# Kernel optimization log

Measured on AMD Instinct MI355X. Metric: run time of the kernel, lower is better.

## Reference

```python
import jax, jax.numpy as jnp
import numpy as np

NUM_QUBITS = 22
NUM_LAYERS = 4
DIM = 2 ** NUM_QUBITS


def _apply_1q(state, U, q):
    # state: flat [2^n]; apply 2x2 unitary U on wire q (wire 0 = most significant)
    s = state.reshape(2 ** q, 2, -1)
    return jnp.einsum('ab,ibj->iaj', U, s).reshape(-1)


def _apply_cnot_adj(state, q):
    # CNOT with control q, target q+1 (adjacent wires)
    s = state.reshape(2 ** q, 2, 2, -1)
    s = jnp.stack([s[:, 0], s[:, 1, ::-1]], axis=1)
    return s.reshape(-1)


def _rot_mats(theta_x, theta_y, theta_z):
    cx = jnp.cos(theta_x / 2).astype(jnp.complex64)
    sx = jnp.sin(theta_x / 2).astype(jnp.complex64)
    RX = jnp.stack([jnp.stack([cx, -1j * sx]), jnp.stack([-1j * sx, cx])])
    cy = jnp.cos(theta_y / 2).astype(jnp.complex64)
    sy = jnp.sin(theta_y / 2).astype(jnp.complex64)
    RY = jnp.stack([jnp.stack([cy, -sy]), jnp.stack([sy, cy])])
    tz = theta_z.astype(jnp.complex64)
    zero = jnp.zeros((), jnp.complex64)
    RZ = jnp.stack([jnp.stack([jnp.exp(-1j * tz / 2), zero]),
                    jnp.stack([zero, jnp.exp(1j * tz / 2)])])
    return RX, RY, RZ


def _circuit(params, state):
    for l in range(NUM_LAYERS):
        for q in range(NUM_QUBITS):
            RX, RY, RZ = _rot_mats(params[l, q, 0], params[l, q, 1], params[l, q, 2])
            state = _apply_1q(state, RX, q)
            state = _apply_1q(state, RY, q)
            state = _apply_1q(state, RZ, q)
        for q in range(NUM_QUBITS - 1):
            state = _apply_cnot_adj(state, q)
    # <Z_q> for each qubit
    probs = jnp.abs(state) ** 2
    expvals = []
    for q in range(NUM_QUBITS):
        p = probs.reshape(2 ** q, 2, -1)
        expvals.append(p[:, 0].sum() - p[:, 1].sum())
    return jnp.stack(expvals).astype(jnp.float32)


def setup_inputs() -> dict:
    key = jax.random.key(0)
    k1, k2, k3 = jax.random.split(key, 3)
    params = jax.random.normal(k1, (NUM_LAYERS, NUM_QUBITS, 3), dtype=jnp.float32)
    state_re = jax.random.normal(k2, (DIM,), dtype=jnp.float32)
    state_im = jax.random.normal(k3, (DIM,), dtype=jnp.float32)
    return {"params": params, "state_re": state_re, "state_im": state_im}


def reference(params, state_re, state_im):
    state = (state_re + 1j * state_im).astype(jnp.complex64)
    state = state / jnp.sqrt(jnp.sum(jnp.abs(state) ** 2))
    return _circuit(params, state)
```

## Files before the change

kernel.cpp:

```cpp
#include <hip/hip_runtime.h>
#include <math.h>

#define NQ 22
#define DIM (1u << NQ)

typedef float v2f __attribute__((ext_vector_type(2)));


__device__ __forceinline__ unsigned igray(unsigned x) {
  x ^= x >> 1; x ^= x >> 2; x ^= x >> 4; x ^= x >> 8; x ^= x >> 16;
  return x;
}

__global__ void k_gates(const float* __restrict__ params, float* __restrict__ U) {
  int t = blockIdx.x * blockDim.x + threadIdx.x;
  if (t >= 88) return;
  const float* p = params + t * 3;
  double hx = 0.5 * (double)p[0], hy = 0.5 * (double)p[1], hz = 0.5 * (double)p[2];
  double cx = cos(hx), sx = sin(hx);
  double cy = cos(hy), sy = sin(hy);
  double cz = cos(hz), sz = sin(hz);
  double m00r = cy * cx, m00i = sy * sx;
  double m01r = -sy * cx, m01i = -cy * sx;
  double m10r = sy * cx, m10i = -cy * sx;
  double m11r = cy * cx, m11i = -sy * sx;
  float* o = U + t * 8;
  o[0] = (float)(cz * m00r + sz * m00i); o[1] = (float)(cz * m00i - sz * m00r);
  o[2] = (float)(cz * m01r + sz * m01i); o[3] = (float)(cz * m01i - sz * m01r);
  o[4] = (float)(cz * m10r - sz * m10i); o[5] = (float)(cz * m10i + sz * m10r);
  o[6] = (float)(cz * m11r - sz * m11i); o[7] = (float)(cz * m11i + sz * m11r);
}

template <int NP>
__device__ __forceinline__ void apply_bit0(v2f RE[NP], v2f IM[NP], const float* __restrict__ u) {
  float u0 = u[0], u1 = u[1], u2 = u[2], u3 = u[3], u4 = u[4], u5 = u[5], u6 = u[6], u7 = u[7];
#pragma unroll
  for (int k = 0; k < NP; ++k) {
    float a0r = RE[k].x, a0i = IM[k].x, a1r = RE[k].y, a1i = IM[k].y;
    float n0r = u0 * a0r - u1 * a0i + u2 * a1r - u3 * a1i;
    float n0i = u0 * a0i + u1 * a0r + u2 * a1i + u3 * a1r;
    float n1r = u4 * a0r - u5 * a0i + u6 * a1r - u7 * a1i;
    float n1i = u4 * a0i + u5 * a0r + u6 * a1i + u7 * a1r;
    RE[k].x = n0r; IM[k].x = n0i; RE[k].y = n1r; IM[k].y = n1i;
  }
}

template <int NP, int PB>
__device__ __forceinline__ void apply_bitP(v2f RE[NP], v2f IM[NP], const float* __restrict__ u) {
  float u0 = u[0], u1 = u[1], u2 = u[2], u3 = u[3], u4 = u[4], u5 = u[5], u6 = u[6], u7 = u[7];
#pragma unroll
  for (int m = 0; m < NP / 2; ++m) {
    int k0 = ((m >> PB) << (PB + 1)) | (m & ((1 << PB) - 1));
    int k1 = k0 | (1 << PB);
    v2f a0r = RE[k0], a0i = IM[k0], a1r = RE[k1], a1i = IM[k1];
    v2f n0r = u0 * a0r - u1 * a0i + u2 * a1r - u3 * a1i;
    v2f n0i = u0 * a0i + u1 * a0r + u2 * a1i + u3 * a1r;
    v2f n1r = u4 * a0r - u5 * a0i + u6 * a1r - u7 * a1i;
    v2f n1i = u4 * a0i + u5 * a0r + u6 * a1i + u7 * a1r;
    RE[k0] = n0r; IM[k0] = n0i; RE[k1] = n1r; IM[k1] = n1i;
  }
}

__device__ __forceinline__ void apply4p(v2f RE[8], v2f IM[8], const float* __restrict__ U,
                                        int l, int wtop) {
  const float* base = U + ((l * 22 + wtop) << 3);
  apply_bit0<8>(RE, IM, base);
  apply_bitP<8, 0>(RE, IM, base - 8);
  apply_bitP<8, 1>(RE, IM, base - 16);
  apply_bitP<8, 2>(RE, IM, base - 24);
}

template <typename WI, typename RI>
__device__ __forceinline__ void xchgP(float2* lds2, v2f RE[8], v2f IM[8], WI wi, RI ri) {
  __syncthreads();
#pragma unroll
  for (int d = 0; d < 16; ++d) {
    float2 a;
    if (d & 1) a = make_float2(RE[d >> 1].y, IM[d >> 1].y);
    else       a = make_float2(RE[d >> 1].x, IM[d >> 1].x);
    lds2[wi(d)] = a;
  }
  __syncthreads();
#pragma unroll
  for (int d = 0; d < 16; ++d) {
    float2 a = lds2[ri(d)];
    if (d & 1) { RE[d >> 1].y = a.x; IM[d >> 1].y = a.y; }
    else       { RE[d >> 1].x = a.x; IM[d >> 1].x = a.y; }
  }
}

__global__ __launch_bounds__(256, 4) void k_passA(const float* __restrict__ srcRe,
                                                  const float* __restrict__ srcIm,
                                                  const float2* __restrict__ src2,
                                                  float2* __restrict__ dst,
                                                  const float* __restrict__ U,
                                                  int layer, int first) {
  __shared__ float2 lds2[4096];
  const int t = threadIdx.x;
  const unsigned bid = blockIdx.x;
  const unsigned H = (bid & 7u) * (gridDim.x >> 3) + (bid >> 3);
  v2f RE[8], IM[8];
  if (first) {
    const unsigned jbase = (H << 12) | ((unsigned)t << 4);
    const float4* r4 = (const float4*)(srcRe + jbase);
    const float4* i4 = (const float4*)(srcIm + jbase);
#pragma unroll
    for (int k = 0; k < 4; ++k) {
      float4 r = r4[k], m = i4[k];
      RE[2 * k].x     = r.x; RE[2 * k].y     = r.y;
      IM[2 * k].x     = m.x; IM[2 * k].y     = m.y;
      RE[2 * k + 1].x = r.z; RE[2 * k + 1].y = r.w;
      IM[2 * k + 1].x = m.z; IM[2 * k + 1].y = m.w;
    }
  } else {
    const float4* s4 = (const float4*)(src2 + (((size_t)H << 12) | ((size_t)t << 4)));
#pragma unroll
    for (int k = 0; k < 8; ++k) {
      float4 a = s4[k];
      RE[k].x = a.x; IM[k].x = a.y;
      RE[k].y = a.z; IM[k].y = a.w;
    }
  }
  auto wA = [&](int d) { unsigned j = ((unsigned)t << 4) | (unsigned)d; return (int)(j ^ (j >> 4)); };
  auto rB = [&](int d) { unsigned j = (((unsigned)t >> 4) << 8) | ((unsigned)d << 4) | ((unsigned)t & 15); return (int)(j ^ (j >> 4)); };
  auto rC = [&](int d) { unsigned j = ((unsigned)d << 8) | (unsigned)t; return (int)(j ^ (j >> 4)); };

  apply4p(RE, IM, U, layer, 21);
  xchgP(lds2, RE, IM, wA, rB);
  apply4p(RE, IM, U, layer, 17);
  xchgP(lds2, RE, IM, rB, rC);
  apply4p(RE, IM, U, layer, 13);
  float2* dp = dst + (((size_t)H << 3) | (unsigned)(t & 7));
#pragma unroll
  for (int d = 0; d < 16; ++d) {
    float2 a;
    if (d & 1) a = make_float2(RE[d >> 1].y, IM[d >> 1].y);
    else       a = make_float2(RE[d >> 1].x, IM[d >> 1].x);
    dp[(((size_t)d << 5) | (unsigned)(t >> 3)) << 13] = a;
  }
}


template <bool EV>
__device__ __forceinline__ void passB_core(const float2* __restrict__ src,
                                           const float* __restrict__ U,
                                           float4* lds4, v2f RE[16], v2f IM[16],
                                           unsigned c2, unsigned u6, unsigned mid,
                                           int layer) {
  const float4* sp4 = (const float4*)src + (((size_t)mid << 12) | c2);
#pragma unroll
  for (int k = 0; k < 16; ++k) {
    float4 a = sp4[((unsigned)k << 8) | (u6 << 2)];
    RE[k].x = a.x; RE[k].y = a.z;
    IM[k].x = a.y; IM[k].y = a.w;
  }
  const float* B = U + layer * 22 * 8;
  apply_bitP<16, 0>(RE, IM, B + 3 * 8);
  apply_bitP<16, 1>(RE, IM, B + 2 * 8);
  apply_bitP<16, 2>(RE, IM, B + 1 * 8);
  apply_bitP<16, 3>(RE, IM, B + 0 * 8);
#pragma unroll
  for (int k = 0; k < 16; ++k) {
    unsigned s = ((unsigned)k << 8) | (u6 << 2) | c2;
    s ^= (s >> 6) & 7u;
    lds4[s] = make_float4(RE[k].x, IM[k].x, RE[k].y, IM[k].y);
  }
  __syncthreads();
#pragma unroll
  for (int k = 0; k < 16; ++k) {
    unsigned s = ((unsigned)k << 2) | (u6 << 6) | c2;
    s ^= (s >> 6) & 7u;
    float4 a = lds4[s];
    RE[k].x = a.x; IM[k].x = a.y;
    RE[k].y = a.z; IM[k].y = a.w;
  }
  apply_bitP<16, 0>(RE, IM, B + 9 * 8);
  apply_bitP<16, 1>(RE, IM, B + 8 * 8);
  apply_bitP<16, 2>(RE, IM, B + 7 * 8);
  apply_bitP<16, 3>(RE, IM, B + 6 * 8);
  __syncthreads();
#pragma unroll
  for (int k = 0; k < 16; ++k) {
    unsigned s = ((unsigned)k << 2) | (u6 << 6) | c2;
    s ^= (s >> 6) & 7u;
    lds4[s] = make_float4(RE[k].x, IM[k].x, RE[k].y, IM[k].y);
  }
  __syncthreads();
#pragma unroll
  for (int k = 0; k < 16; ++k) {
    unsigned h = (u6 & 15u) | (((unsigned)k & 3u) << 4) | (((unsigned)k >> 2) << 6) | ((u6 >> 4) << 8);
    unsigned s = (h << 2) | c2;
    s ^= (s >> 6) & 7u;
    float4 a = lds4[s];
    RE[k].x = a.x; IM[k].x = a.y;
    RE[k].y = a.z; IM[k].y = a.w;
  }
  apply_bitP<16, 0>(RE, IM, B + 5 * 8);
  apply_bitP<16, 1>(RE, IM, B + 4 * 8);
}

__global__ __launch_bounds__(256, 2) void k_passB(const float2* __restrict__ src,
                                                  float2* __restrict__ dst,
                                                  const float* __restrict__ U,
                                                  int layer) {
  __shared__ float4 lds4[4096];
  const int t = threadIdx.x;
  const unsigned c2 = (unsigned)(t & 3), u6 = (unsigned)(t >> 2);
  const unsigned bid = blockIdx.x;
  const unsigned mid = (bid & 7u) * (gridDim.x >> 3) + (bid >> 3);
  v2f RE[16], IM[16];
  passB_core<false>(src, U, lds4, RE, IM, c2, u6, mid, layer);
  const unsigned Tb = igray(((u6 & 15u) << 12) | ((u6 >> 4) << 20) | (mid << 3) | (c2 << 1));
  float4* dp4 = (float4*)dst;
#pragma unroll
  for (int k = 0; k < 16; ++k) {
    unsigned a2 = Tb ^ igray((((unsigned)k & 3u) << 16) | (((unsigned)k >> 2) << 18));
    float4 v = (a2 & 1u) ? make_float4(RE[k].y, IM[k].y, RE[k].x, IM[k].x)
                         : make_float4(RE[k].x, IM[k].x, RE[k].y, IM[k].y);
    dp4[a2 >> 1] = v;
  }
}

__global__ __launch_bounds__(256, 2) void k_passB_ev(const float2* __restrict__ src,
                                                     const float* __restrict__ U,
                                                     float* __restrict__ partials,
                                                     int layer) {
  __shared__ float4 lds4[4096];
  const int t = threadIdx.x;
  const unsigned c2 = (unsigned)(t & 3), u6 = (unsigned)(t >> 2);
  const unsigned bid = blockIdx.x;
  const unsigned mid = (bid & 7u) * (gridDim.x >> 3) + (bid >> 3);
  v2f RE[16], IM[16];
  passB_core<true>(src, U, lds4, RE, IM, c2, u6, mid, layer);

  v2f PS[16];
#pragma unroll
  for (int k = 0; k < 16; ++k) PS[k] = RE[k] * RE[k] + IM[k] * IM[k];
  float Tot = 0.f, WA = 0.f;
  v2f B4[8];
#pragma unroll
  for (int k = 0; k < 8; ++k) {
    v2f S = PS[k] + PS[k + 8];
    Tot += S.x + S.y;
    B4[k] = PS[k] - PS[k + 8];
    WA += B4[k].x + B4[k].y;
  }
  v2f B3[4];
  float WB = 0.f;
#pragma unroll
  for (int k = 0; k < 4; ++k) {
    B3[k] = B4[k] - B4[k + 4];
    WB += B3[k].x + B3[k].y;
  }
  v2f B2[2];
  B2[0] = B3[0] - B3[2]; B2[1] = B3[1] - B3[3];
  float WC = (B2[0].x + B2[0].y) + (B2[1].x + B2[1].y);
  v2f B1 = B2[0] - B2[1];
  float W4 = B1.x + B1.y;
  float W5 = B1.x - B1.y;

  unsigned lowT = (mid << 3) | (c2 << 1);
  unsigned y = lowT; y ^= y >> 1; y ^= y >> 2; y ^= y >> 4; y ^= y >> 8;
  unsigned pu = (unsigned)__popc(u6) & 1u;
  float acc[22];
  acc[0] = ((u6 >> 5) & 1u) ? -Tot : Tot;
  {
    unsigned s01 = (unsigned)__popc(u6 >> 4) & 1u;
    acc[1] = s01 ? -Tot : Tot;
    float sg = s01 ? -1.f : 1.f;
    acc[2] = sg * WA; acc[3] = sg * WB; acc[4] = sg * WC; acc[5] = sg * W4;
  }
#pragma unroll
  for (int q = 6; q <= 9; ++q)
    acc[q] = ((unsigned)__popc(u6 >> (9 - q)) & 1u) ? -W4 : W4;
#pragma unroll
  for (int q = 10; q <= 20; ++q)
    acc[q] = (((y >> (21 - q)) ^ pu) & 1u) ? -W4 : W4;
  acc[21] = (((y >> 1) ^ pu) & 1u) ? -W5 : W5;

  __syncthreads();
  float* red = (float*)lds4;
  const int lane = t & 63, wv = t >> 6;
#pragma unroll
  for (int q = 0; q < 22; ++q) {
    float s = acc[q];
    for (int off = 32; off > 0; off >>= 1) s += __shfl_down(s, off, 64);
    if (lane == 0) red[wv * 23 + q] = s;
  }
  {
    float s = Tot;
    for (int off = 32; off > 0; off >>= 1) s += __shfl_down(s, off, 64);
    if (lane == 0) red[wv * 23 + 22] = s;
  }
  __syncthreads();
  if (t < 23) {
    float s = 0.f;
#pragma unroll
    for (int w = 0; w < 4; ++w) s += red[w * 23 + t];
    partials[t * 512 + mid] = s;
  }
}

__global__ void k_final(const float* __restrict__ partials, float* __restrict__ out) {
  __shared__ double res[32];
  const int t = threadIdx.x;
  const int r = t >> 3, l8 = t & 7;
  if (r < 23) {
    double s = 0.0;
    const float* p = partials + r * 512 + l8 * 64;
    for (int k = 0; k < 64; ++k) s += (double)p[k];
    for (int off = 4; off > 0; off >>= 1) s += __shfl_down(s, off, 8);
    if (l8 == 0) res[r] = s;
  }
  __syncthreads();
  if (t < 22) out[t] = (float)(res[t] / res[22]);
}

extern "C" void kernel_launch(void* const* d_in, const int* in_sizes, int n_in,
                              void* d_out, int out_size, void* d_ws, size_t ws_size,
                              hipStream_t stream) {
  const float* params = (const float*)d_in[0];
  const float* sre = (const float*)d_in[1];
  const float* sim = (const float*)d_in[2];
  float* out = (float*)d_out;
  char* ws = (char*)d_ws;
  float* U = (float*)ws;
  float* partials = (float*)(ws + 4096);
  float2* buf0 = (float2*)(ws + 131072);
  float2* buf1 = buf0 + DIM;

  k_gates<<<1, 128, 0, stream>>>(params, U);
  k_passA<<<1024, 256, 0, stream>>>(sre, sim, nullptr, buf0, U, 0, 1);
  k_passB<<<512, 256, 0, stream>>>(buf0, buf1, U, 0);
  for (int l = 1; l < 3; ++l) {
    k_passA<<<1024, 256, 0, stream>>>(nullptr, nullptr, buf1, buf0, U, l, 0);
    k_passB<<<512, 256, 0, stream>>>(buf0, buf1, U, l);
  }
  k_passA<<<1024, 256, 0, stream>>>(nullptr, nullptr, buf1, buf0, U, 3, 0);
  k_passB_ev<<<512, 256, 0, stream>>>(buf0, U, partials, 3);
  k_final<<<1, 256, 0, stream>>>(partials, out);
}
```

Baseline: 206.9 us.

## Restructure passB into smaller 8-amplitude-per-thread tiles with more blocks

Pass B now handles 10 qubits per block in 3-bit stages, with each thread holding 8 amplitude pairs instead of 16. Shared memory halves to 32KB per block, the grid doubles to 1024 blocks and launch bounds allow 4 blocks per CU. The goal is more occupancy and latency hiding for this memory-bound pass. The cost is an extra LDS exchange round with its own syncs, a reworked XOR swizzle, recomputed expectation-value sign bookkeeping, and twice as many partial sums for the final reduction.

```diff
diff --git a/kernel.cpp b/kernel.cpp
--- a/kernel.cpp
+++ b/kernel.cpp
@@ -141,142 +141,125 @@
 }
 
 
-template <bool EV>
-__device__ __forceinline__ void passB_core(const float2* __restrict__ src,
-                                           const float* __restrict__ U,
-                                           float4* lds4, v2f RE[16], v2f IM[16],
-                                           unsigned c2, unsigned u6, unsigned mid,
-                                           int layer) {
-  const float4* sp4 = (const float4*)src + (((size_t)mid << 12) | c2);
-#pragma unroll
-  for (int k = 0; k < 16; ++k) {
-    float4 a = sp4[((unsigned)k << 8) | (u6 << 2)];
-    RE[k].x = a.x; RE[k].y = a.z;
-    IM[k].x = a.y; IM[k].y = a.w;
-  }
-  const float* B = U + layer * 22 * 8;
-  apply_bitP<16, 0>(RE, IM, B + 3 * 8);
-  apply_bitP<16, 1>(RE, IM, B + 2 * 8);
-  apply_bitP<16, 2>(RE, IM, B + 1 * 8);
-  apply_bitP<16, 3>(RE, IM, B + 0 * 8);
-#pragma unroll
-  for (int k = 0; k < 16; ++k) {
-    unsigned s = ((unsigned)k << 8) | (u6 << 2) | c2;
-    s ^= (s >> 6) & 7u;
-    lds4[s] = make_float4(RE[k].x, IM[k].x, RE[k].y, IM[k].y);
-  }
-  __syncthreads();
-#pragma unroll
-  for (int k = 0; k < 16; ++k) {
-    unsigned s = ((unsigned)k << 2) | (u6 << 6) | c2;
-    s ^= (s >> 6) & 7u;
-    float4 a = lds4[s];
-    RE[k].x = a.x; IM[k].x = a.y;
-    RE[k].y = a.z; IM[k].y = a.w;
-  }
-  apply_bitP<16, 0>(RE, IM, B + 9 * 8);
-  apply_bitP<16, 1>(RE, IM, B + 8 * 8);
-  apply_bitP<16, 2>(RE, IM, B + 7 * 8);
-  apply_bitP<16, 3>(RE, IM, B + 6 * 8);
-  __syncthreads();
-#pragma unroll
-  for (int k = 0; k < 16; ++k) {
-    unsigned s = ((unsigned)k << 2) | (u6 << 6) | c2;
-    s ^= (s >> 6) & 7u;
-    lds4[s] = make_float4(RE[k].x, IM[k].x, RE[k].y, IM[k].y);
-  }
-  __syncthreads();
-#pragma unroll
-  for (int k = 0; k < 16; ++k) {
-    unsigned h = (u6 & 15u) | (((unsigned)k & 3u) << 4) | (((unsigned)k >> 2) << 6) | ((u6 >> 4) << 8);
-    unsigned s = (h << 2) | c2;
-    s ^= (s >> 6) & 7u;
-    float4 a = lds4[s];
-    RE[k].x = a.x; IM[k].x = a.y;
-    RE[k].y = a.z; IM[k].y = a.w;
-  }
-  apply_bitP<16, 0>(RE, IM, B + 5 * 8);
-  apply_bitP<16, 1>(RE, IM, B + 4 * 8);
-}
-
-__global__ __launch_bounds__(256, 2) void k_passB(const float2* __restrict__ src,
+__device__ __forceinline__ int phi(unsigned o) {
+  return (int)(o ^ (((o >> 4) & 7u) << 1));
+}
+
+template <typename WI, typename RI>
+__device__ __forceinline__ void xch4(float4* L, v2f RE[8], v2f IM[8], WI wi, RI ri) {
+#pragma unroll
+  for (int k = 0; k < 8; ++k)
+    L[wi(k)] = make_float4(RE[k].x, IM[k].x, RE[k].y, IM[k].y);
+  __syncthreads();
+#pragma unroll
+  for (int k = 0; k < 8; ++k) {
+    float4 a = L[ri(k)];
+    RE[k].x = a.x; IM[k].x = a.y; RE[k].y = a.z; IM[k].y = a.w;
+  }
+  __syncthreads();
+}
+
+__device__ __forceinline__ void passB_core5(const float2* __restrict__ src,
+                                            const float* __restrict__ B,
+                                            float4* lds4, v2f RE[8], v2f IM[8],
+                                            unsigned c1, unsigned u7,
+                                            unsigned mid, unsigned a2) {
+  const float4* sp4 = (const float4*)src + (((size_t)mid << 12) | (u7 << 2) | (a2 << 1) | c1);
+#pragma unroll
+  for (int k = 0; k < 8; ++k) {
+    float4 a = sp4[(unsigned)k << 9];
+    RE[k].x = a.x; IM[k].x = a.y; RE[k].y = a.z; IM[k].y = a.w;
+  }
+  apply_bitP<8, 0>(RE, IM, B + 2 * 8);
+  apply_bitP<8, 1>(RE, IM, B + 1 * 8);
+  apply_bitP<8, 2>(RE, IM, B + 0 * 8);
+  auto w1 = [&](int k) { return phi(((((unsigned)k << 7) | u7) << 1) | c1); };
+  auto r1 = [&](int k) { return phi((((u7 << 3) | (unsigned)k) << 1) | c1); };
+  xch4(lds4, RE, IM, w1, r1);
+  apply_bitP<8, 0>(RE, IM, B + 9 * 8);
+  apply_bitP<8, 1>(RE, IM, B + 8 * 8);
+  apply_bitP<8, 2>(RE, IM, B + 7 * 8);
+  auto r2 = [&](int k) { return phi((((u7 & 7u) | ((unsigned)k << 3) | ((u7 >> 3) << 6)) << 1) | c1); };
+  xch4(lds4, RE, IM, r1, r2);
+  apply_bitP<8, 0>(RE, IM, B + 6 * 8);
+  apply_bitP<8, 1>(RE, IM, B + 5 * 8);
+  apply_bitP<8, 2>(RE, IM, B + 4 * 8);
+  auto r3 = [&](int k) { return phi((((u7 & 63u) | ((unsigned)k << 6) | ((u7 >> 6) << 9)) << 1) | c1); };
+  xch4(lds4, RE, IM, r2, r3);
+  apply_bitP<8, 0>(RE, IM, B + 3 * 8);
+}
+
+__global__ __launch_bounds__(256, 4) void k_passB(const float2* __restrict__ src,
                                                   float2* __restrict__ dst,
                                                   const float* __restrict__ U,
                                                   int layer) {
-  __shared__ float4 lds4[4096];
+  __shared__ float4 lds4[2048];
   const int t = threadIdx.x;
-  const unsigned c2 = (unsigned)(t & 3), u6 = (unsigned)(t >> 2);
+  const unsigned c1 = (unsigned)(t & 1), u7 = (unsigned)(t >> 1);
   const unsigned bid = blockIdx.x;
-  const unsigned mid = (bid & 7u) * (gridDim.x >> 3) + (bid >> 3);
-  v2f RE[16], IM[16];
-  passB_core<false>(src, U, lds4, RE, IM, c2, u6, mid, layer);
-  const unsigned Tb = igray(((u6 & 15u) << 12) | ((u6 >> 4) << 20) | (mid << 3) | (c2 << 1));
+  const unsigned H = (bid & 7u) * (gridDim.x >> 3) + (bid >> 3);
+  const unsigned mid = H >> 1, a2 = H & 1u;
+  v2f RE[8], IM[8];
+  passB_core5(src, U + layer * 22 * 8, lds4, RE, IM, c1, u7, mid, a2);
+  const unsigned Tb = igray(((u7 & 63u) << 12) | ((u7 >> 6) << 21) |
+                            (mid << 3) | (a2 << 2) | (c1 << 1));
   float4* dp4 = (float4*)dst;
 #pragma unroll
-  for (int k = 0; k < 16; ++k) {
-    unsigned a2 = Tb ^ igray((((unsigned)k & 3u) << 16) | (((unsigned)k >> 2) << 18));
-    float4 v = (a2 & 1u) ? make_float4(RE[k].y, IM[k].y, RE[k].x, IM[k].x)
-                         : make_float4(RE[k].x, IM[k].x, RE[k].y, IM[k].y);
-    dp4[a2 >> 1] = v;
-  }
-}
-
-__global__ __launch_bounds__(256, 2) void k_passB_ev(const float2* __restrict__ src,
+  for (int k = 0; k < 8; ++k) {
+    unsigned a2x = Tb ^ igray((unsigned)k << 18);
+    float4 v = (a2x & 1u) ? make_float4(RE[k].y, IM[k].y, RE[k].x, IM[k].x)
+                          : make_float4(RE[k].x, IM[k].x, RE[k].y, IM[k].y);
+    dp4[a2x >> 1] = v;
+  }
+}
+
+__global__ __launch_bounds__(256, 4) void k_passB_ev(const float2* __restrict__ src,
                                                      const float* __restrict__ U,
                                                      float* __restrict__ partials,
                                                      int layer) {
-  __shared__ float4 lds4[4096];
+  __shared__ float4 lds4[2048];
   const int t = threadIdx.x;
-  const unsigned c2 = (unsigned)(t & 3), u6 = (unsigned)(t >> 2);
+  const unsigned c1 = (unsigned)(t & 1), u7 = (unsigned)(t >> 1);
   const unsigned bid = blockIdx.x;
-  const unsigned mid = (bid & 7u) * (gridDim.x >> 3) + (bid >> 3);
-  v2f RE[16], IM[16];
-  passB_core<true>(src, U, lds4, RE, IM, c2, u6, mid, layer);
-
-  v2f PS[16];
-#pragma unroll
-  for (int k = 0; k < 16; ++k) PS[k] = RE[k] * RE[k] + IM[k] * IM[k];
-  float Tot = 0.f, WA = 0.f;
-  v2f B4[8];
-#pragma unroll
-  for (int k = 0; k < 8; ++k) {
-    v2f S = PS[k] + PS[k + 8];
+  const unsigned H = (bid & 7u) * (gridDim.x >> 3) + (bid >> 3);
+  const unsigned mid = H >> 1, a2 = H & 1u;
+  v2f RE[8], IM[8];
+  passB_core5(src, U + layer * 22 * 8, lds4, RE, IM, c1, u7, mid, a2);
+
+  v2f PS[8];
+#pragma unroll
+  for (int k = 0; k < 8; ++k) PS[k] = RE[k] * RE[k] + IM[k] * IM[k];
+  float Tot = 0.f, W20 = 0.f;
+  v2f Ba[4];
+#pragma unroll
+  for (int j = 0; j < 4; ++j) {
+    v2f S = PS[j] + PS[j + 4];
     Tot += S.x + S.y;
-    B4[k] = PS[k] - PS[k + 8];
-    WA += B4[k].x + B4[k].y;
-  }
-  v2f B3[4];
-  float WB = 0.f;
-#pragma unroll
-  for (int k = 0; k < 4; ++k) {
-    B3[k] = B4[k] - B4[k + 4];
-    WB += B3[k].x + B3[k].y;
-  }
-  v2f B2[2];
-  B2[0] = B3[0] - B3[2]; B2[1] = B3[1] - B3[3];
-  float WC = (B2[0].x + B2[0].y) + (B2[1].x + B2[1].y);
-  v2f B1 = B2[0] - B2[1];
-  float W4 = B1.x + B1.y;
-  float W5 = B1.x - B1.y;
-
-  unsigned lowT = (mid << 3) | (c2 << 1);
-  unsigned y = lowT; y ^= y >> 1; y ^= y >> 2; y ^= y >> 4; y ^= y >> 8;
-  unsigned pu = (unsigned)__popc(u6) & 1u;
+    Ba[j] = PS[j] - PS[j + 4];
+    W20 += Ba[j].x + Ba[j].y;
+  }
+  v2f Bb0 = Ba[0] - Ba[2], Bb1 = Ba[1] - Ba[3];
+  float W19 = Bb0.x + Bb0.y + Bb1.x + Bb1.y;
+  v2f Bc = Bb0 - Bb1;
+  float Wk = Bc.x + Bc.y;
+  float Wkb = Bc.x - Bc.y;
+
+  const unsigned s21 = (u7 >> 6) & 1u;
+  const unsigned pu6 = (unsigned)__popc(u7 & 63u) & 1u;
+  unsigned low = (mid << 3) | (a2 << 2) | (c1 << 1);
+  unsigned y = low; y ^= y >> 1; y ^= y >> 2; y ^= y >> 4; y ^= y >> 8;
   float acc[22];
-  acc[0] = ((u6 >> 5) & 1u) ? -Tot : Tot;
   {
-    unsigned s01 = (unsigned)__popc(u6 >> 4) & 1u;
-    acc[1] = s01 ? -Tot : Tot;
-    float sg = s01 ? -1.f : 1.f;
-    acc[2] = sg * WA; acc[3] = sg * WB; acc[4] = sg * WC; acc[5] = sg * W4;
-  }
-#pragma unroll
-  for (int q = 6; q <= 9; ++q)
-    acc[q] = ((unsigned)__popc(u6 >> (9 - q)) & 1u) ? -W4 : W4;
-#pragma unroll
-  for (int q = 10; q <= 20; ++q)
-    acc[q] = (((y >> (21 - q)) ^ pu) & 1u) ? -W4 : W4;
-  acc[21] = (((y >> 1) ^ pu) & 1u) ? -W5 : W5;
+    float sg = s21 ? -1.f : 1.f;
+    acc[0] = sg * Tot; acc[1] = sg * W20; acc[2] = sg * W19; acc[3] = sg * Wk;
+  }
+#pragma unroll
+  for (int q = 4; q <= 8; ++q)
+    acc[q] = (((unsigned)__popc((u7 & 63u) >> (9 - q)) ^ s21) & 1u) ? -Wk : Wk;
+#pragma unroll
+  for (int q = 9; q <= 20; ++q)
+    acc[q] = (((y >> (21 - q)) ^ s21 ^ pu6) & 1u) ? -Wk : Wk;
+  acc[21] = ((y ^ s21 ^ pu6) & 1u) ? -Wkb : Wkb;
 
   __syncthreads();
   float* red = (float*)lds4;
@@ -297,7 +280,7 @@
     float s = 0.f;
 #pragma unroll
     for (int w = 0; w < 4; ++w) s += red[w * 23 + t];
-    partials[t * 512 + mid] = s;
+    partials[t * 1024 + ((mid << 1) | a2)] = s;
   }
 }
 
@@ -307,8 +290,8 @@
   const int r = t >> 3, l8 = t & 7;
   if (r < 23) {
     double s = 0.0;
-    const float* p = partials + r * 512 + l8 * 64;
-    for (int k = 0; k < 64; ++k) s += (double)p[k];
+    const float* p = partials + r * 1024 + l8 * 128;
+    for (int k = 0; k < 128; ++k) s += (double)p[k];
     for (int off = 4; off > 0; off >>= 1) s += __shfl_down(s, off, 8);
     if (l8 == 0) res[r] = s;
   }
@@ -331,12 +314,12 @@
 
   k_gates<<<1, 128, 0, stream>>>(params, U);
   k_passA<<<1024, 256, 0, stream>>>(sre, sim, nullptr, buf0, U, 0, 1);
-  k_passB<<<512, 256, 0, stream>>>(buf0, buf1, U, 0);
+  k_passB<<<1024, 256, 0, stream>>>(buf0, buf1, U, 0);
   for (int l = 1; l < 3; ++l) {
     k_passA<<<1024, 256, 0, stream>>>(nullptr, nullptr, buf1, buf0, U, l, 0);
-    k_passB<<<512, 256, 0, stream>>>(buf0, buf1, U, l);
+    k_passB<<<1024, 256, 0, stream>>>(buf0, buf1, U, l);
   }
   k_passA<<<1024, 256, 0, stream>>>(nullptr, nullptr, buf1, buf0, U, 3, 0);
-  k_passB_ev<<<512, 256, 0, stream>>>(buf0, U, partials, 3);
+  k_passB_ev<<<1024, 256, 0, stream>>>(buf0, U, partials, 3);
   k_final<<<1, 256, 0, stream>>>(partials, out);
 }
```

After: 217.1 us. 4.9% more time.
